# Kernel optimization log

Measured on AMD Instinct MI355X. Metric: run time of the kernel, lower is better.

## Reference

```python
import jax, jax.numpy as jnp
import numpy as np

B, S, H = 1, 2048, 1024          # batch, seq_len, hidden_dim
E, I = 16, 512                    # num_experts, moe_intermediate_size
TOP_K = 4
NORM_TOPK_PROB = True


def setup_inputs() -> dict:
    key = jax.random.key(0)
    k0, k1, k2, k3, k4 = jax.random.split(key, 5)
    scale = 0.02
    return {
        "hidden_states": jax.random.normal(k0, (B, S, H), jnp.float32),
        "w_gate": jax.random.normal(k1, (H, E), jnp.float32) * scale,
        "w_gate_proj": jax.random.normal(k2, (E, H, I), jnp.float32) * scale,
        "w_up_proj": jax.random.normal(k3, (E, H, I), jnp.float32) * scale,
        "w_down_proj": jax.random.normal(k4, (E, I, H), jnp.float32) * scale,
    }


def reference(hidden_states, w_gate, w_gate_proj, w_up_proj, w_down_proj):
    b, s, h = hidden_states.shape
    x = hidden_states.reshape(-1, h)                      # [T, H]
    T = x.shape[0]

    router_logits = x @ w_gate                            # [T, E]
    routing_weights = jax.nn.softmax(router_logits.astype(jnp.float32), axis=-1)
    top_w, sel = jax.lax.top_k(routing_weights, TOP_K)    # [T, K]
    if NORM_TOPK_PROB:
        top_w = top_w / top_w.sum(axis=-1, keepdims=True)
    top_w = top_w.astype(x.dtype)

    # Per-token combine weight for every expert (0 if not in top-k).
    # Mathematically identical to the sort/gather/index_add dispatch loop.
    combine = jnp.zeros((T, E), x.dtype).at[
        jnp.arange(T)[:, None], sel].set(top_w)           # [T, E]

    def expert_step(acc, inp):
        wg, wu, wd, w = inp                               # [H,I],[H,I],[I,H],[T]
        hidden = jax.nn.silu(x @ wg) * (x @ wu)           # [T, I]
        return acc + (hidden @ wd) * w[:, None], None

    out0 = jnp.zeros_like(x)
    out, _ = jax.lax.scan(
        expert_step, out0,
        (w_gate_proj, w_up_proj, w_down_proj, combine.T))
    return out.reshape(b, s, h), router_logits
```

## Files before the change

### kernel.cpp

```cpp
#include <hip/hip_runtime.h>
#include <math.h>

constexpr int TT = 2048;
constexpr int HH = 1024;
constexpr int EE = 16;
constexpr int II = 512;

typedef unsigned short u16;
typedef short s16x8 __attribute__((ext_vector_type(8)));
typedef float f32x4 __attribute__((ext_vector_type(4)));

__device__ __forceinline__ u16 f2bf(float f) {
  unsigned u = __float_as_uint(f);
  u = (u + 0x7fffu + ((u >> 16) & 1u)) >> 16;
  return (u16)u;
}
__device__ __forceinline__ float bf2f(u16 b) {
  return __uint_as_float(((unsigned)b) << 16);
}

__device__ __forceinline__ void gl2lds16(const void* g, void* l) {
  __builtin_amdgcn_global_load_lds(
      (const __attribute__((address_space(1))) unsigned*)g,
      (__attribute__((address_space(3))) unsigned*)l, 16, 0, 0);
}

__global__ __launch_bounds__(256) void prep_kernel(
    const float* __restrict__ wgp, const float* __restrict__ wup,
    const float* __restrict__ wdp, u16* __restrict__ wgt,
    u16* __restrict__ wut, u16* __restrict__ wdt,
    const float* __restrict__ x, u16* __restrict__ xb,
    const float* __restrict__ wg, float* __restrict__ wgT) {
  int bid = blockIdx.x;
  int tid = threadIdx.x;
  if (bid < 12288) {
    int z = bid >> 8, lb = bid & 255;
    int e = z & 15, t = z >> 4;
    const float* src; u16* dst; int K, N;
    if (t == 0)      { src = wgp + (size_t)e * HH * II; dst = wgt + (size_t)e * II * HH; K = HH; N = II; }
    else if (t == 1) { src = wup + (size_t)e * HH * II; dst = wut + (size_t)e * II * HH; K = HH; N = II; }
    else             { src = wdp + (size_t)e * II * HH; dst = wdt + (size_t)e * HH * II; K = II; N = HH; }
    int nTiles = N >> 6;
    int n0 = (lb % nTiles) * 64;
    int k0 = (lb / nTiles) * 32;
    int l = tid & 63, w = tid >> 6;
    int n  = n0 + w * 16 + (l >> 2);
    int kc = l & 3;
    float v[8];
#pragma unroll
    for (int j = 0; j < 8; ++j)
      v[j] = src[(size_t)(k0 + kc * 8 + j) * N + n];
    uint4 st;
    st.x = (unsigned)f2bf(v[0]) | ((unsigned)f2bf(v[1]) << 16);
    st.y = (unsigned)f2bf(v[2]) | ((unsigned)f2bf(v[3]) << 16);
    st.z = (unsigned)f2bf(v[4]) | ((unsigned)f2bf(v[5]) << 16);
    st.w = (unsigned)f2bf(v[6]) | ((unsigned)f2bf(v[7]) << 16);
    *reinterpret_cast<uint4*>(&dst[(size_t)n * K + k0 + kc * 8]) = st;
  } else if (bid < 12288 + 2048) {
    int i = (bid - 12288) * 256 + tid;
    float4 v = reinterpret_cast<const float4*>(x)[i];
    ushort4 o;
    o.x = f2bf(v.x); o.y = f2bf(v.y); o.z = f2bf(v.z); o.w = f2bf(v.w);
    reinterpret_cast<ushort4*>(xb)[i] = o;
  } else {
    int i = (bid - 12288 - 2048) * 256 + tid;
    int h = i >> 4, e = i & 15;
    wgT[e * HH + h] = wg[i];
  }
}

__global__ void router_kernel(const float* __restrict__ x, const float* __restrict__ wgT,
                              float* __restrict__ rl, unsigned* __restrict__ selmask,
                              float* __restrict__ wsel) {
  int lane = threadIdx.x & 63, wv = threadIdx.x >> 6;
  int t = blockIdx.x * 4 + wv;
  const float* xr = x + (size_t)t * HH;
  float xv[16];
#pragma unroll
  for (int i = 0; i < 16; ++i) xv[i] = xr[lane + 64 * i];
  float lg[16];
#pragma unroll
  for (int e = 0; e < 16; ++e) {
    const float* wr = wgT + (size_t)e * HH;
    float p = 0.f;
#pragma unroll
    for (int i = 0; i < 16; ++i) p += xv[i] * wr[lane + 64 * i];
#pragma unroll
    for (int s = 32; s > 0; s >>= 1) p += __shfl_xor(p, s, 64);
    lg[e] = p;
  }
  if (lane < 16) rl[(size_t)t * 16 + lane] = lg[lane];
  unsigned mask = 0;
  int sel[4]; float bl[4];
#pragma unroll
  for (int k = 0; k < 4; ++k) {
    float best = -3.4e38f; int bi = 0;
#pragma unroll
    for (int e = 0; e < 16; ++e) {
      bool ok = !((mask >> e) & 1u) && (lg[e] > best);
      best = ok ? lg[e] : best;
      bi = ok ? e : bi;
    }
    mask |= 1u << bi;
    sel[k] = bi; bl[k] = best;
  }
  float mx = bl[0];
  float wk[4]; float s = 0.f;
#pragma unroll
  for (int k = 0; k < 4; ++k) { wk[k] = expf(bl[k] - mx); s += wk[k]; }
  float inv = 1.f / s;
  if (lane == 0) {
    selmask[t] = (unsigned)sel[0] | ((unsigned)sel[1] << 4) |
                 ((unsigned)sel[2] << 8) | ((unsigned)sel[3] << 12);
    float4 w4 = make_float4(wk[0] * inv, wk[1] * inv, wk[2] * inv, wk[3] * inv);
    reinterpret_cast<float4*>(wsel)[t] = w4;
  }
}

__global__ void build_lists_kernel(const unsigned* __restrict__ selmask,
                                   const float* __restrict__ wsel,
                                   int* __restrict__ counts, int* __restrict__ offsets,
                                   int* __restrict__ tlist, float* __restrict__ wlist,
                                   int* __restrict__ rowof) {
  __shared__ int scnt[16];
  __shared__ int soff[16];
  int lane = threadIdx.x & 63, e = threadIdx.x >> 6;
  int base = 0;
  for (int t0 = 0; t0 < TT; t0 += 64) {
    unsigned m = selmask[t0 + lane];
    bool hit = false;
#pragma unroll
    for (int j = 0; j < 4; ++j)
      hit |= (((m >> (4 * j)) & 15u) == (unsigned)e);
    base += (int)__popcll(__ballot(hit));
  }
  if (lane == 0) scnt[e] = base;
  __syncthreads();
  if (threadIdx.x == 0) {
    int s = 0;
    for (int i = 0; i < 16; ++i) { counts[i] = scnt[i]; offsets[i] = s; soff[i] = s; s += scnt[i]; }
    offsets[16] = s;
  }
  __syncthreads();
  int hb = soff[e];
  base = 0;
  for (int t0 = 0; t0 < TT; t0 += 64) {
    int t = t0 + lane;
    unsigned m = selmask[t];
    int k = -1;
#pragma unroll
    for (int j = 0; j < 4; ++j)
      if (((m >> (4 * j)) & 15u) == (unsigned)e) k = j;
    unsigned long long bal = __ballot(k >= 0);
    int pos = base + (int)__popcll(bal & ((1ull << lane) - 1ull));
    if (k >= 0) {
      tlist[e * TT + pos] = t;
      wlist[e * TT + pos] = wsel[t * 4 + k];
      rowof[t * 4 + k] = hb + pos;
    }
    base += (int)__popcll(bal);
  }
}

__global__ __launch_bounds__(256, 2) void gateup_kernel(
    const u16* __restrict__ xb, const u16* __restrict__ wgt, const u16* __restrict__ wut,
    const int* __restrict__ counts, const int* __restrict__ offsets,
    const int* __restrict__ tlist, const float* __restrict__ wlist,
    u16* __restrict__ hidden) {
  int e = blockIdx.z, mt = blockIdx.y, nt = blockIdx.x;
  int cnt = counts[e];
  if (mt * 128 >= cnt) return;
  __shared__ u16 As[128 * 64];
  __shared__ u16 Bg[64 * 64];
  __shared__ u16 Bu[64 * 64];
  int tid = threadIdx.x, lane = tid & 63, wv = tid >> 6;
  int wm = wv >> 1, wn = wv & 1;
  int srow = lane >> 3;
  int scol = (((lane & 7) ^ srow)) * 8;
  const u16* wgE = wgt + (size_t)e * II * HH;
  const u16* wuE = wut + (size_t)e * II * HH;
  const u16* gp[8];
#pragma unroll
  for (int c = 0; c < 8; ++c) {
    int chunk = c * 4 + wv;
    const u16* p;
    if (chunk < 16) {
      int mi = mt * 128 + chunk * 8 + srow; if (mi >= cnt) mi = cnt - 1;
      int tok = tlist[e * TT + mi];
      p = xb + (size_t)tok * HH + scol;
    } else if (chunk < 24) {
      int n = nt * 64 + (chunk - 16) * 8 + srow;
      p = wgE + (size_t)n * HH + scol;
    } else {
      int n = nt * 64 + (chunk - 24) * 8 + srow;
      p = wuE + (size_t)n * HH + scol;
    }
    gp[c] = p;
  }
  f32x4 accG[4][2] = {}; f32x4 accU[4][2] = {};
  int quad = lane >> 4, colc = lane & 15;
  for (int k0 = 0; k0 < HH; k0 += 64) {
#pragma unroll
    for (int c = 0; c < 8; ++c) {
      int chunk = c * 4 + wv;
      u16* dst = (chunk < 16) ? &As[chunk * 512]
               : (chunk < 24) ? &Bg[(chunk - 16) * 512]
                              : &Bu[(chunk - 24) * 512];
      gl2lds16(gp[c] + k0, dst);
    }
    __syncthreads();
#pragma unroll
    for (int kk = 0; kk < 64; kk += 32) {
      int gl = (kk >> 3) + quad;
      s16x8 a[4], bg[2], bu[2];
#pragma unroll
      for (int f = 0; f < 4; ++f) {
        int m = wm * 64 + f * 16 + colc;
        a[f] = *reinterpret_cast<const s16x8*>(&As[m * 64 + ((gl ^ (m & 7)) << 3)]);
      }
#pragma unroll
      for (int f = 0; f < 2; ++f) {
        int n = wn * 32 + f * 16 + colc;
        bg[f] = *reinterpret_cast<const s16x8*>(&Bg[n * 64 + ((gl ^ (n & 7)) << 3)]);
        bu[f] = *reinterpret_cast<const s16x8*>(&Bu[n * 64 + ((gl ^ (n & 7)) << 3)]);
      }
#pragma unroll
      for (int fm = 0; fm < 4; ++fm)
#pragma unroll
        for (int fn = 0; fn < 2; ++fn) {
          accG[fm][fn] = __builtin_amdgcn_mfma_f32_16x16x32_bf16(a[fm], bg[fn], accG[fm][fn], 0, 0, 0);
          accU[fm][fn] = __builtin_amdgcn_mfma_f32_16x16x32_bf16(a[fm], bu[fn], accU[fm][fn], 0, 0, 0);
        }
    }
    __syncthreads();
  }
  int hb = offsets[e];
#pragma unroll
  for (int fm = 0; fm < 4; ++fm) {
#pragma unroll
    for (int r = 0; r < 4; ++r) {
      int mi = mt * 128 + wm * 64 + fm * 16 + quad * 4 + r;
      if (mi < cnt) {
        float wr = wlist[e * TT + mi];
        u16* hrow = hidden + (size_t)(hb + mi) * II + nt * 64 + wn * 32;
#pragma unroll
        for (int fn = 0; fn < 2; ++fn) {
          float g = accG[fm][fn][r], u = accU[fm][fn][r];
          float hval = wr * u * g / (1.f + expf(-g));
          hrow[fn * 16 + colc] = f2bf(hval);
        }
      }
    }
  }
}

__global__ __launch_bounds__(256, 2) void down_kernel(
    const u16* __restrict__ hidden, const u16* __restrict__ wdt,
    const int* __restrict__ counts, const int* __restrict__ offsets,
    u16* __restrict__ dtmp) {
  int e = blockIdx.z, mt = blockIdx.y, nt = blockIdx.x;
  int cnt = counts[e];
  if (mt * 128 >= cnt) return;
  int hb = offsets[e];
  __shared__ u16 As[128 * 64];
  __shared__ u16 Bs[128 * 64];
  int tid = threadIdx.x, lane = tid & 63, wv = tid >> 6;
  int wm = wv >> 1, wn = wv & 1;
  int srow = lane >> 3;
  int scol = (((lane & 7) ^ srow)) * 8;
  const u16* wdE = wdt + (size_t)e * HH * II;
  const u16* gA[4]; const u16* gB[4];
#pragma unroll
  for (int c = 0; c < 4; ++c) {
    int chunk = c * 4 + wv;
    int row = hb + mt * 128 + chunk * 8 + srow;
    if (row > 8191) row = 8191;
    gA[c] = hidden + (size_t)row * II + scol;
    int n = nt * 128 + chunk * 8 + srow;
    gB[c] = wdE + (size_t)n * II + scol;
  }
  f32x4 acc[4][4] = {};
  int quad = lane >> 4, colc = lane & 15;
  for (int k0 = 0; k0 < II; k0 += 64) {
#pragma unroll
    for (int c = 0; c < 4; ++c) {
      int chunk = c * 4 + wv;
      gl2lds16(gA[c] + k0, &As[chunk * 512]);
      gl2lds16(gB[c] + k0, &Bs[chunk * 512]);
    }
    __syncthreads();
#pragma unroll
    for (int kk = 0; kk < 64; kk += 32) {
      int gl = (kk >> 3) + quad;
      s16x8 a[4], b[4];
#pragma unroll
      for (int f = 0; f < 4; ++f) {
        int m = wm * 64 + f * 16 + colc;
        int n = wn * 64 + f * 16 + colc;
        a[f] = *reinterpret_cast<const s16x8*>(&As[m * 64 + ((gl ^ (m & 7)) << 3)]);
        b[f] = *reinterpret_cast<const s16x8*>(&Bs[n * 64 + ((gl ^ (n & 7)) << 3)]);
      }
#pragma unroll
      for (int fm = 0; fm < 4; ++fm)
#pragma unroll
        for (int fn = 0; fn < 4; ++fn)
          acc[fm][fn] = __builtin_amdgcn_mfma_f32_16x16x32_bf16(a[fm], b[fn], acc[fm][fn], 0, 0, 0);
    }
    __syncthreads();
  }
#pragma unroll
  for (int fm = 0; fm < 4; ++fm) {
#pragma unroll
    for (int r = 0; r < 4; ++r) {
      int mi = mt * 128 + wm * 64 + fm * 16 + quad * 4 + r;
      if (mi < cnt) {
        u16* drow = dtmp + (size_t)(hb + mi) * HH + nt * 128 + wn * 64;
#pragma unroll
        for (int fn = 0; fn < 4; ++fn)
          drow[fn * 16 + colc] = f2bf(acc[fm][fn][r]);
      }
    }
  }
}

__global__ void combine_kernel(const u16* __restrict__ dtmp, const int* __restrict__ rowof,
                               float* __restrict__ out) {
  int t = blockIdx.x, tid = threadIdx.x;
  int4 rw = reinterpret_cast<const int4*>(rowof)[t];
  int h = tid * 4;
  float s0 = 0.f, s1 = 0.f, s2 = 0.f, s3 = 0.f;
  int rows[4] = {rw.x, rw.y, rw.z, rw.w};
#pragma unroll
  for (int k = 0; k < 4; ++k) {
    ushort4 v = *reinterpret_cast<const ushort4*>(&dtmp[(size_t)rows[k] * HH + h]);
    s0 += bf2f(v.x); s1 += bf2f(v.y); s2 += bf2f(v.z); s3 += bf2f(v.w);
  }
  *reinterpret_cast<float4*>(&out[(size_t)t * HH + h]) = make_float4(s0, s1, s2, s3);
}

extern "C" void kernel_launch(void* const* d_in, const int* in_sizes, int n_in,
                              void* d_out, int out_size, void* d_ws, size_t ws_size,
                              hipStream_t stream) {
  const float* x   = (const float*)d_in[0];
  const float* wg  = (const float*)d_in[1];
  const float* wgp = (const float*)d_in[2];
  const float* wup = (const float*)d_in[3];
  const float* wdp = (const float*)d_in[4];
  float* out = (float*)d_out;
  float* rl  = out + (size_t)TT * HH;

  char* w = (char*)d_ws;
  int*      counts  = (int*)(w + 0);
  int*      offsets = (int*)(w + 64);
  unsigned* selmask = (unsigned*)(w + 1024);
  float*    wsel    = (float*)(w + 16384);
  int*      rowof   = (int*)(w + 49152);
  int*      tlist   = (int*)(w + 81920);
  float*    wlist   = (float*)(w + 210944);
  float*    wgT     = (float*)(w + 339968);
  u16*      xb      = (u16*)(w + 405504);
  u16*      wgt     = xb  + (size_t)TT * HH;
  u16*      wut     = wgt + (size_t)EE * II * HH;
  u16*      wdt     = wut + (size_t)EE * II * HH;
  u16*      hidden  = wdt + (size_t)EE * HH * II;
  u16*      dtmp    = wgt;

  hipLaunchKernelGGL(prep_kernel, dim3(12288 + 2048 + 64), dim3(256), 0, stream,
                     wgp, wup, wdp, wgt, wut, wdt, x, xb, wg, wgT);
  hipLaunchKernelGGL(router_kernel, dim3(TT / 4), dim3(256), 0, stream,
                     x, wgT, rl, selmask, wsel);
  hipLaunchKernelGGL(build_lists_kernel, dim3(1), dim3(1024), 0, stream,
                     selmask, wsel, counts, offsets, tlist, wlist, rowof);
  hipLaunchKernelGGL(gateup_kernel, dim3(8, 16, 16), dim3(256), 0, stream,
                     xb, wgt, wut, counts, offsets, tlist, wlist, hidden);
  hipLaunchKernelGGL(down_kernel, dim3(8, 16, 16), dim3(256), 0, stream,
                     hidden, wdt, counts, offsets, dtmp);
  hipLaunchKernelGGL(combine_kernel, dim3(TT), dim3(256), 0, stream,
                     dtmp, rowof, out);
}
```

Before: 231.2 us.

## Fuse router and dispatch-list construction into prep kernel using atomics

Moves the router (logits, top-k, softmax) into the first blocks of the prep kernel, reading w_gate directly as float4 rows instead of a transposed copy. The single-block build_lists kernel is replaced with per-token atomicAdd slot assignment into fixed per-expert regions (e*TT), so prefix offsets are no longer needed. This removes two kernel launches and a serial single-block pass, at the cost of a memset, nondeterministic token order within each expert, and a larger fixed-stride workspace layout.

```diff
diff --git a/kernel.cpp b/kernel.cpp
--- a/kernel.cpp
+++ b/kernel.cpp
@@ -30,11 +30,71 @@
     const float* __restrict__ wdp, u16* __restrict__ wgt,
     u16* __restrict__ wut, u16* __restrict__ wdt,
     const float* __restrict__ x, u16* __restrict__ xb,
-    const float* __restrict__ wg, float* __restrict__ wgT) {
+    const float* __restrict__ wg, float* __restrict__ rl,
+    int* __restrict__ counts, int* __restrict__ tlist,
+    float* __restrict__ wlist, int* __restrict__ rowof) {
   int bid = blockIdx.x;
   int tid = threadIdx.x;
-  if (bid < 12288) {
-    int z = bid >> 8, lb = bid & 255;
+  if (bid < 512) {
+    int lane = tid & 63, wv = tid >> 6;
+    int t = bid * 4 + wv;
+    const float* xr = x + (size_t)t * HH;
+    float xv[16];
+#pragma unroll
+    for (int i = 0; i < 16; ++i) xv[i] = xr[lane + 64 * i];
+    float lg[16];
+#pragma unroll
+    for (int e = 0; e < 16; ++e) lg[e] = 0.f;
+#pragma unroll
+    for (int i = 0; i < 16; ++i) {
+      const float4* wr = reinterpret_cast<const float4*>(wg + (size_t)(lane + 64 * i) * EE);
+      float4 w0 = wr[0], w1 = wr[1], w2 = wr[2], w3 = wr[3];
+      float xs = xv[i];
+      lg[0]  += xs * w0.x; lg[1]  += xs * w0.y; lg[2]  += xs * w0.z; lg[3]  += xs * w0.w;
+      lg[4]  += xs * w1.x; lg[5]  += xs * w1.y; lg[6]  += xs * w1.z; lg[7]  += xs * w1.w;
+      lg[8]  += xs * w2.x; lg[9]  += xs * w2.y; lg[10] += xs * w2.z; lg[11] += xs * w2.w;
+      lg[12] += xs * w3.x; lg[13] += xs * w3.y; lg[14] += xs * w3.z; lg[15] += xs * w3.w;
+    }
+#pragma unroll
+    for (int e = 0; e < 16; ++e) {
+      float p = lg[e];
+#pragma unroll
+      for (int s = 32; s > 0; s >>= 1) p += __shfl_xor(p, s, 64);
+      lg[e] = p;
+    }
+    if (lane < 16) rl[(size_t)t * 16 + lane] = lg[lane];
+    unsigned mask = 0;
+    int sel[4]; float bl[4];
+#pragma unroll
+    for (int k = 0; k < 4; ++k) {
+      float best = -3.4e38f; int bi = 0;
+#pragma unroll
+      for (int e = 0; e < 16; ++e) {
+        bool ok = !((mask >> e) & 1u) && (lg[e] > best);
+        best = ok ? lg[e] : best;
+        bi = ok ? e : bi;
+      }
+      mask |= 1u << bi;
+      sel[k] = bi; bl[k] = best;
+    }
+    float mx = bl[0];
+    float wk[4]; float s = 0.f;
+#pragma unroll
+    for (int k = 0; k < 4; ++k) { wk[k] = expf(bl[k] - mx); s += wk[k]; }
+    float inv = 1.f / s;
+    if (lane == 0) {
+#pragma unroll
+      for (int k = 0; k < 4; ++k) {
+        int e = sel[k];
+        int pos = atomicAdd(&counts[e * 16], 1);
+        tlist[e * TT + pos] = t;
+        wlist[e * TT + pos] = wk[k] * inv;
+        rowof[t * 4 + k] = e * TT + pos;
+      }
+    }
+  } else if (bid < 512 + 12288) {
+    int b = bid - 512;
+    int z = b >> 8, lb = b & 255;
     int e = z & 15, t = z >> 4;
     const float* src; u16* dst; int K, N;
     if (t == 0)      { src = wgp + (size_t)e * HH * II; dst = wgt + (size_t)e * II * HH; K = HH; N = II; }
@@ -56,119 +116,22 @@
     st.z = (unsigned)f2bf(v[4]) | ((unsigned)f2bf(v[5]) << 16);
     st.w = (unsigned)f2bf(v[6]) | ((unsigned)f2bf(v[7]) << 16);
     *reinterpret_cast<uint4*>(&dst[(size_t)n * K + k0 + kc * 8]) = st;
-  } else if (bid < 12288 + 2048) {
-    int i = (bid - 12288) * 256 + tid;
+  } else {
+    int i = (bid - 12800) * 256 + tid;
     float4 v = reinterpret_cast<const float4*>(x)[i];
     ushort4 o;
     o.x = f2bf(v.x); o.y = f2bf(v.y); o.z = f2bf(v.z); o.w = f2bf(v.w);
     reinterpret_cast<ushort4*>(xb)[i] = o;
-  } else {
-    int i = (bid - 12288 - 2048) * 256 + tid;
-    int h = i >> 4, e = i & 15;
-    wgT[e * HH + h] = wg[i];
-  }
-}
-
-__global__ void router_kernel(const float* __restrict__ x, const float* __restrict__ wgT,
-                              float* __restrict__ rl, unsigned* __restrict__ selmask,
-                              float* __restrict__ wsel) {
-  int lane = threadIdx.x & 63, wv = threadIdx.x >> 6;
-  int t = blockIdx.x * 4 + wv;
-  const float* xr = x + (size_t)t * HH;
-  float xv[16];
-#pragma unroll
-  for (int i = 0; i < 16; ++i) xv[i] = xr[lane + 64 * i];
-  float lg[16];
-#pragma unroll
-  for (int e = 0; e < 16; ++e) {
-    const float* wr = wgT + (size_t)e * HH;
-    float p = 0.f;
-#pragma unroll
-    for (int i = 0; i < 16; ++i) p += xv[i] * wr[lane + 64 * i];
-#pragma unroll
-    for (int s = 32; s > 0; s >>= 1) p += __shfl_xor(p, s, 64);
-    lg[e] = p;
-  }
-  if (lane < 16) rl[(size_t)t * 16 + lane] = lg[lane];
-  unsigned mask = 0;
-  int sel[4]; float bl[4];
-#pragma unroll
-  for (int k = 0; k < 4; ++k) {
-    float best = -3.4e38f; int bi = 0;
-#pragma unroll
-    for (int e = 0; e < 16; ++e) {
-      bool ok = !((mask >> e) & 1u) && (lg[e] > best);
-      best = ok ? lg[e] : best;
-      bi = ok ? e : bi;
-    }
-    mask |= 1u << bi;
-    sel[k] = bi; bl[k] = best;
-  }
-  float mx = bl[0];
-  float wk[4]; float s = 0.f;
-#pragma unroll
-  for (int k = 0; k < 4; ++k) { wk[k] = expf(bl[k] - mx); s += wk[k]; }
-  float inv = 1.f / s;
-  if (lane == 0) {
-    selmask[t] = (unsigned)sel[0] | ((unsigned)sel[1] << 4) |
-                 ((unsigned)sel[2] << 8) | ((unsigned)sel[3] << 12);
-    float4 w4 = make_float4(wk[0] * inv, wk[1] * inv, wk[2] * inv, wk[3] * inv);
-    reinterpret_cast<float4*>(wsel)[t] = w4;
-  }
-}
-
-__global__ void build_lists_kernel(const unsigned* __restrict__ selmask,
-                                   const float* __restrict__ wsel,
-                                   int* __restrict__ counts, int* __restrict__ offsets,
-                                   int* __restrict__ tlist, float* __restrict__ wlist,
-                                   int* __restrict__ rowof) {
-  __shared__ int scnt[16];
-  __shared__ int soff[16];
-  int lane = threadIdx.x & 63, e = threadIdx.x >> 6;
-  int base = 0;
-  for (int t0 = 0; t0 < TT; t0 += 64) {
-    unsigned m = selmask[t0 + lane];
-    bool hit = false;
-#pragma unroll
-    for (int j = 0; j < 4; ++j)
-      hit |= (((m >> (4 * j)) & 15u) == (unsigned)e);
-    base += (int)__popcll(__ballot(hit));
-  }
-  if (lane == 0) scnt[e] = base;
-  __syncthreads();
-  if (threadIdx.x == 0) {
-    int s = 0;
-    for (int i = 0; i < 16; ++i) { counts[i] = scnt[i]; offsets[i] = s; soff[i] = s; s += scnt[i]; }
-    offsets[16] = s;
-  }
-  __syncthreads();
-  int hb = soff[e];
-  base = 0;
-  for (int t0 = 0; t0 < TT; t0 += 64) {
-    int t = t0 + lane;
-    unsigned m = selmask[t];
-    int k = -1;
-#pragma unroll
-    for (int j = 0; j < 4; ++j)
-      if (((m >> (4 * j)) & 15u) == (unsigned)e) k = j;
-    unsigned long long bal = __ballot(k >= 0);
-    int pos = base + (int)__popcll(bal & ((1ull << lane) - 1ull));
-    if (k >= 0) {
-      tlist[e * TT + pos] = t;
-      wlist[e * TT + pos] = wsel[t * 4 + k];
-      rowof[t * 4 + k] = hb + pos;
-    }
-    base += (int)__popcll(bal);
   }
 }
 
 __global__ __launch_bounds__(256, 2) void gateup_kernel(
     const u16* __restrict__ xb, const u16* __restrict__ wgt, const u16* __restrict__ wut,
-    const int* __restrict__ counts, const int* __restrict__ offsets,
+    const int* __restrict__ counts,
     const int* __restrict__ tlist, const float* __restrict__ wlist,
     u16* __restrict__ hidden) {
   int e = blockIdx.z, mt = blockIdx.y, nt = blockIdx.x;
-  int cnt = counts[e];
+  int cnt = counts[e * 16];
   if (mt * 128 >= cnt) return;
   __shared__ u16 As[128 * 64];
   __shared__ u16 Bg[64 * 64];
@@ -234,7 +197,7 @@
     }
     __syncthreads();
   }
-  int hb = offsets[e];
+  int hb = e * TT;
 #pragma unroll
   for (int fm = 0; fm < 4; ++fm) {
 #pragma unroll
@@ -256,12 +219,12 @@
 
 __global__ __launch_bounds__(256, 2) void down_kernel(
     const u16* __restrict__ hidden, const u16* __restrict__ wdt,
-    const int* __restrict__ counts, const int* __restrict__ offsets,
+    const int* __restrict__ counts,
     u16* __restrict__ dtmp) {
   int e = blockIdx.z, mt = blockIdx.y, nt = blockIdx.x;
-  int cnt = counts[e];
+  int cnt = counts[e * 16];
   if (mt * 128 >= cnt) return;
-  int hb = offsets[e];
+  int hb = e * TT;
   __shared__ u16 As[128 * 64];
   __shared__ u16 Bs[128 * 64];
   int tid = threadIdx.x, lane = tid & 63, wv = tid >> 6;
@@ -274,7 +237,6 @@
   for (int c = 0; c < 4; ++c) {
     int chunk = c * 4 + wv;
     int row = hb + mt * 128 + chunk * 8 + srow;
-    if (row > 8191) row = 8191;
     gA[c] = hidden + (size_t)row * II + scol;
     int n = nt * 128 + chunk * 8 + srow;
     gB[c] = wdE + (size_t)n * II + scol;
@@ -349,32 +311,27 @@
   float* out = (float*)d_out;
   float* rl  = out + (size_t)TT * HH;
 
+  constexpr size_t MB = 1048576;
   char* w = (char*)d_ws;
   int*      counts  = (int*)(w + 0);
-  int*      offsets = (int*)(w + 64);
-  unsigned* selmask = (unsigned*)(w + 1024);
-  float*    wsel    = (float*)(w + 16384);
-  int*      rowof   = (int*)(w + 49152);
-  int*      tlist   = (int*)(w + 81920);
-  float*    wlist   = (float*)(w + 210944);
-  float*    wgT     = (float*)(w + 339968);
-  u16*      xb      = (u16*)(w + 405504);
-  u16*      wgt     = xb  + (size_t)TT * HH;
-  u16*      wut     = wgt + (size_t)EE * II * HH;
-  u16*      wdt     = wut + (size_t)EE * II * HH;
-  u16*      hidden  = wdt + (size_t)EE * HH * II;
-  u16*      dtmp    = wgt;
-
-  hipLaunchKernelGGL(prep_kernel, dim3(12288 + 2048 + 64), dim3(256), 0, stream,
-                     wgp, wup, wdp, wgt, wut, wdt, x, xb, wg, wgT);
-  hipLaunchKernelGGL(router_kernel, dim3(TT / 4), dim3(256), 0, stream,
-                     x, wgT, rl, selmask, wsel);
-  hipLaunchKernelGGL(build_lists_kernel, dim3(1), dim3(1024), 0, stream,
-                     selmask, wsel, counts, offsets, tlist, wlist, rowof);
+  int*      rowof   = (int*)(w + 4096);
+  int*      tlist   = (int*)(w + 65536);
+  float*    wlist   = (float*)(w + 65536 + 131072);
+  u16*      xb      = (u16*)(w + 1 * MB);
+  u16*      wgt     = (u16*)(w + 8 * MB);
+  u16*      wut     = (u16*)(w + 24 * MB);
+  u16*      wdt     = (u16*)(w + 40 * MB);
+  u16*      hidden  = (u16*)(w + 56 * MB);
+  u16*      dtmp    = (u16*)(w + 96 * MB);
+
+  hipMemsetAsync(counts, 0, 1024, stream);
+  hipLaunchKernelGGL(prep_kernel, dim3(512 + 12288 + 2048), dim3(256), 0, stream,
+                     wgp, wup, wdp, wgt, wut, wdt, x, xb, wg, rl,
+                     counts, tlist, wlist, rowof);
   hipLaunchKernelGGL(gateup_kernel, dim3(8, 16, 16), dim3(256), 0, stream,
-                     xb, wgt, wut, counts, offsets, tlist, wlist, hidden);
+                     xb, wgt, wut, counts, tlist, wlist, hidden);
   hipLaunchKernelGGL(down_kernel, dim3(8, 16, 16), dim3(256), 0, stream,
-                     hidden, wdt, counts, offsets, dtmp);
+                     hidden, wdt, counts, dtmp);
   hipLaunchKernelGGL(combine_kernel, dim3(TT), dim3(256), 0, stream,
                      dtmp, rowof, out);
 }
```

Result: faster. 212.3 us (-8.2%).
